# Performance work log

Measured on AMD Instinct MI355X. Metric: run time of the kernel, lower is better.

The kernel has to match this reference:

```python
import jax, jax.numpy as jnp
import numpy as np

STRIDE = 1
PADDING = (1, 1, 1, 1)  # (left, right, top, bottom), as in torch F.pad for last two dims
NEG_INF = -jnp.inf


def maxplus_conv2d(x, kernel, stride=STRIDE):
    """Tropical (max-plus) conv2d, groups=1.
    x: [B, C, H, W] (already padded), kernel: [O, C, kh, kw].
    out[b,o,h,w] = max_{c,ki,kj} x[b,c,h*s+ki,w*s+kj] + kernel[o,c,ki,kj]
    """
    B, C, H, W = x.shape
    O, Cg, kh, kw = kernel.shape
    Ho = (H - kh) // stride + 1
    Wo = (W - kw) // stride + 1
    out = jnp.full((B, O, Ho, Wo), NEG_INF, dtype=x.dtype)
    # Loop over the small, fixed kernel taps (kh*kw = 9); reductions over the
    # channel axis stay fully vectorized and fuse into a single add+reduce-max.
    for ki in range(kh):
        for kj in range(kw):
            xs = x[:, :, ki:ki + Ho * stride:stride, kj:kj + Wo * stride:stride]  # [B,C,Ho,Wo]
            cand = jnp.max(xs[:, None, :, :, :] + kernel[None, :, :, ki, kj][:, :, :, None, None], axis=2)
            out = jnp.maximum(out, cand)
    return out


def setup_inputs() -> dict:
    key = jax.random.key(0)
    kx, kk = jax.random.split(key)
    x = jax.random.normal(kx, (8, 64, 64, 64), dtype=jnp.float32)
    kernel = jax.random.normal(kk, (64, 64, 3, 3), dtype=jnp.float32) * 0.1
    return {"x": x, "kernel": kernel}


def reference(x, kernel):
    left, right, top, bottom = PADDING
    # MaxPlus semifield: pad with the additive identity of max, i.e. -inf
    xp = jnp.pad(x, ((0, 0), (0, 0), (top, bottom), (left, right)), mode="constant", constant_values=NEG_INF)
    return maxplus_conv2d(xp, kernel, STRIDE)
```

## Files before the change

### kernel.cpp

```cpp
#include <hip/hip_runtime.h>

#define NEG_INF (-__builtin_huge_valf())
#define NEG_INF_BITS 0xFF800000

#define CCH   4
#define HB    4
#define ROWS  (HB + 2)
#define XSTR  64
#define SLOTS 6

template <int CTRL>
__device__ __forceinline__ float dpp_neighbor(float v) {
    return __int_as_float(__builtin_amdgcn_update_dpp(
        (int)NEG_INF_BITS, __float_as_int(v), CTRL, 0xF, 0xF, false));
}

__global__ __launch_bounds__(64, 4)
void maxplus_conv2d_kernel(const float* __restrict__ x,
                           const float* __restrict__ kern,
                           float* __restrict__ out) {
    __shared__ float xs[CCH * ROWS * XSTR];

    const int tid = threadIdx.x;
    const int wg  = tid & 15;
    const int hr  = tid >> 4;
    const int w0  = wg << 2;

    const int h_base = blockIdx.x * HB;
    const int b      = blockIdx.y;
    const int o_base = blockIdx.z << 1;

    const float* xb = x + (size_t)b * 64 * 64 * 64;
    const float* gsrc[SLOTS];
    float*       xdst[SLOTS];
    bool         vmask[SLOTS];
#pragma unroll
    for (int k = 0; k < SLOTS; ++k) {
        int rowid = k * 4 + hr;
        int cl    = rowid / ROWS;
        int r     = rowid - cl * ROWS;
        int gh    = h_base + r - 1;
        bool valid = (unsigned)gh < 64u;
        int  ghc   = valid ? gh : 0;
        gsrc[k]  = xb + ((size_t)cl * 64 + ghc) * 64 + wg * 4;
        xdst[k]  = &xs[rowid * XSTR + wg * 4];
        vmask[k] = valid;
    }

    float acc[2][4];
#pragma unroll
    for (int oo = 0; oo < 2; ++oo)
#pragma unroll
        for (int wi = 0; wi < 4; ++wi)
            acc[oo][wi] = NEG_INF;

    float4 R[SLOTS];
#pragma unroll
    for (int k = 0; k < SLOTS; ++k) R[k] = *(const float4*)gsrc[k];

#pragma unroll 1
    for (int cc = 0; cc < 64; cc += CCH) {
        __syncthreads();

#pragma unroll
        for (int k = 0; k < SLOTS; ++k) {
            float4 v = R[k];
            if (!vmask[k]) v = make_float4(NEG_INF, NEG_INF, NEG_INF, NEG_INF);
            *(float4*)xdst[k] = v;
        }

        __syncthreads();

        if (cc + CCH < 64) {
#pragma unroll
            for (int k = 0; k < SLOTS; ++k) {
                gsrc[k] += CCH * 64 * 64;
                R[k] = *(const float4*)gsrc[k];
            }
        }

        float kv[CCH][2][9];
#pragma unroll
        for (int cl = 0; cl < CCH; ++cl)
#pragma unroll
            for (int oo = 0; oo < 2; ++oo) {
                const float* kp = kern + ((size_t)(o_base + oo) * 64 + (cc + cl)) * 9;
#pragma unroll
                for (int t = 0; t < 9; ++t) kv[cl][oo][t] = kp[t];
            }

#pragma unroll
        for (int cl = 0; cl < CCH; ++cl) {
            float xv[3][6];
#pragma unroll
            for (int r = 0; r < 3; ++r) {
                const int rowid = cl * ROWS + hr + r;
                float4 m = *(const float4*)(&xs[rowid * XSTR + w0]);
                xv[r][0] = dpp_neighbor<0x111>(m.w);
                xv[r][1] = m.x; xv[r][2] = m.y; xv[r][3] = m.z; xv[r][4] = m.w;
                xv[r][5] = dpp_neighbor<0x101>(m.x);
            }

#pragma unroll
            for (int oo = 0; oo < 2; ++oo) {
                const float* k9 = kv[cl][oo];
#pragma unroll
                for (int wi = 0; wi < 4; ++wi) {
                    float m = acc[oo][wi];
                    float t0 = xv[0][wi + 0] + k9[0];
                    float t1 = xv[0][wi + 1] + k9[1];
                    m = fmaxf(m, fmaxf(t0, t1));
                    t0 = xv[0][wi + 2] + k9[2];
                    t1 = xv[1][wi + 0] + k9[3];
                    m = fmaxf(m, fmaxf(t0, t1));
                    t0 = xv[1][wi + 1] + k9[4];
                    t1 = xv[1][wi + 2] + k9[5];
                    m = fmaxf(m, fmaxf(t0, t1));
                    t0 = xv[2][wi + 0] + k9[6];
                    t1 = xv[2][wi + 1] + k9[7];
                    m = fmaxf(m, fmaxf(t0, t1));
                    m = fmaxf(m, xv[2][wi + 2] + k9[8]);
                    acc[oo][wi] = m;
                }
            }
        }
    }

    const int h = h_base + hr;
#pragma unroll
    for (int oo = 0; oo < 2; ++oo) {
        float4 v = make_float4(acc[oo][0], acc[oo][1], acc[oo][2], acc[oo][3]);
        *(float4*)(out + ((((size_t)b * 64 + (o_base + oo)) * 64 + h) * 64 + w0)) = v;
    }
}

extern "C" void kernel_launch(void* const* d_in, const int* in_sizes, int n_in,
                              void* d_out, int out_size, void* d_ws, size_t ws_size,
                              hipStream_t stream) {
    const float* x    = (const float*)d_in[0];
    const float* kern = (const float*)d_in[1];
    float* out = (float*)d_out;

    dim3 grid(16, 8, 32);
    dim3 block(64);
    maxplus_conv2d_kernel<<<grid, block, 0, stream>>>(x, kern, out);
}
```

Measured before the change: 121.2 us.

## Stage kernel weights in LDS and double-buffer shared-memory row reads

Preloads the block's two output channels' 3x3 weights for all 64 input channels into LDS once at kernel start, padded to a stride of 12. This replaces the per-iteration global (scalar) weight loads. It also prefetches the next channel's three input rows from LDS into registers while the current channel is computed, to hide LDS latency. The cost is extra LDS usage (about 6 KB), which may reduce occupancy, plus more register pressure from the double buffer.

```diff
diff --git a/kernel.cpp b/kernel.cpp
--- a/kernel.cpp
+++ b/kernel.cpp
@@ -8,6 +8,7 @@
 #define ROWS  (HB + 2)
 #define XSTR  64
 #define SLOTS 6
+#define KSTR  12
 
 template <int CTRL>
 __device__ __forceinline__ float dpp_neighbor(float v) {
@@ -20,6 +21,7 @@
                            const float* __restrict__ kern,
                            float* __restrict__ out) {
     __shared__ float xs[CCH * ROWS * XSTR];
+    __shared__ float klds[2 * 64 * KSTR];
 
     const int tid = threadIdx.x;
     const int wg  = tid & 15;
@@ -29,6 +31,20 @@
     const int h_base = blockIdx.x * HB;
     const int b      = blockIdx.y;
     const int o_base = blockIdx.z << 1;
+
+    {
+        const float* kb = kern + (size_t)o_base * 576;
+#pragma unroll
+        for (int i = 0; i < 24; ++i) {
+            int idx = i * 64 + tid;
+            int oo  = idx / 768;
+            int rem = idx - oo * 768;
+            int c   = rem / KSTR;
+            int t   = rem - c * KSTR;
+            int ts  = t < 9 ? t : 8;
+            klds[idx] = kb[oo * 576 + c * 9 + ts];
+        }
+    }
 
     const float* xb = x + (size_t)b * 64 * 64 * 64;
     const float* gsrc[SLOTS];
@@ -79,23 +95,34 @@
             }
         }
 
-        float kv[CCH][2][9];
+        float4 xr[2][3];
 #pragma unroll
-        for (int cl = 0; cl < CCH; ++cl)
-#pragma unroll
-            for (int oo = 0; oo < 2; ++oo) {
-                const float* kp = kern + ((size_t)(o_base + oo) * 64 + (cc + cl)) * 9;
-#pragma unroll
-                for (int t = 0; t < 9; ++t) kv[cl][oo][t] = kp[t];
-            }
+        for (int r = 0; r < 3; ++r)
+            xr[0][r] = *(const float4*)(&xs[(0 * ROWS + hr + r) * XSTR + w0]);
 
 #pragma unroll
         for (int cl = 0; cl < CCH; ++cl) {
+            const int cur = cl & 1;
+
+            float kr[2][9];
+#pragma unroll
+            for (int oo = 0; oo < 2; ++oo) {
+                const float* kp = &klds[(oo * 64 + cc + cl) * KSTR];
+#pragma unroll
+                for (int t = 0; t < 9; ++t) kr[oo][t] = kp[t];
+            }
+
+            if (cl + 1 < CCH) {
+#pragma unroll
+                for (int r = 0; r < 3; ++r)
+                    xr[cur ^ 1][r] = *(const float4*)(
+                        &xs[((cl + 1) * ROWS + hr + r) * XSTR + w0]);
+            }
+
             float xv[3][6];
 #pragma unroll
             for (int r = 0; r < 3; ++r) {
-                const int rowid = cl * ROWS + hr + r;
-                float4 m = *(const float4*)(&xs[rowid * XSTR + w0]);
+                float4 m = xr[cur][r];
                 xv[r][0] = dpp_neighbor<0x111>(m.w);
                 xv[r][1] = m.x; xv[r][2] = m.y; xv[r][3] = m.z; xv[r][4] = m.w;
                 xv[r][5] = dpp_neighbor<0x101>(m.x);
@@ -103,7 +130,7 @@
 
 #pragma unroll
             for (int oo = 0; oo < 2; ++oo) {
-                const float* k9 = kv[cl][oo];
+                const float* k9 = kr[oo];
 #pragma unroll
                 for (int wi = 0; wi < 4; ++wi) {
                     float m = acc[oo][wi];
```

New measurement: 138.1 us. 13.9% more time.
